# Kernel tuning notes

Measured on AMD Instinct MI355X. Metric: run time of the kernel, lower is better.

The kernel has to match this reference:

```python
import jax, jax.numpy as jnp
import numpy as np

N, DX, D, K, H = 4096, 128, 64, 256, 256
BETA = 0.25


def setup_inputs() -> dict:
    key = jax.random.key(0)
    ks = jax.random.split(key, 10)
    z_sample = jax.random.normal(ks[0], (N, D), jnp.float32)
    k_idx = jax.random.randint(ks[1], (N,), 0, K)
    k_sample = jax.nn.one_hot(k_idx, K, dtype=jnp.float32)  # carry is one-hot
    xt = jax.random.normal(ks[2], (N, DX), jnp.float32)
    mask = jax.random.bernoulli(ks[3], 0.5, (N,))
    transition = jax.random.uniform(ks[4], (N, K, K), jnp.float32, 0.01, 1.0)
    start_pk = jax.random.uniform(ks[5], (N, K), jnp.float32, 0.01, 1.0)
    start_pk = start_pk / start_pk.sum(-1, keepdims=True)
    W1 = jax.random.normal(ks[6], (D + DX, H), jnp.float32) / np.float32(np.sqrt(D + DX))
    b1 = jnp.zeros((H,), jnp.float32)
    W2 = jax.random.normal(ks[7], (H, H), jnp.float32) / np.float32(np.sqrt(H))
    b2 = jnp.zeros((H,), jnp.float32)
    W3 = jax.random.normal(ks[8], (H, D), jnp.float32) / np.float32(np.sqrt(H))
    b3 = jnp.zeros((D,), jnp.float32)
    C = jax.random.normal(ks[9], (K, D), jnp.float32)
    return dict(temp=jnp.float32(1.0), z_sample=z_sample, k_sample=k_sample, xt=xt,
                mask=mask, transition=transition, start_pk=start_pk,
                W1=W1, b1=b1, W2=W2, b2=b2, W3=W3, b3=b3, C=C, seed=0)


def reference(temp, z_sample, k_sample, xt, mask, transition, start_pk,
              W1, b1, W2, b2, W3, b3, C, seed):
    key = jax.random.key(seed)
    k_rng, z_rng, key = jax.random.split(key, 3)

    # replace non-finite carry entries (initial-step sentinel)
    zf = jnp.where(jnp.isfinite(z_sample), z_sample, jnp.zeros_like(z_sample))
    kf = jnp.where(jnp.isfinite(k_sample), k_sample, jnp.ones_like(k_sample))

    # SmallTanhNet encoder gt = ez([z, x])
    h = jnp.tanh(jnp.concatenate([zf, xt], axis=-1) @ W1 + b1)
    h = jnp.tanh(h @ W2 + b2)
    gt = h @ W3 + b3  # [N, D]

    # codebook pairwise Euclidean distance + argmin (VQ)
    diff = gt[:, None, :] - C[None, :, :]  # [N, K, D]
    distances = jnp.sqrt(jnp.sum(diff * diff, axis=-1))  # [N, K]
    qk_ind = jnp.argmin(distances, axis=-1)
    qk_sample = jax.nn.one_hot(qk_ind, K, dtype=gt.dtype)  # [N, K]

    # prior over discrete state from per-sample transition
    pk_gammat = jnp.einsum('nk,nkj->nj', kf, transition)
    pk_gammat = pk_gammat / pk_gammat.sum(axis=-1, keepdims=True)
    pk_gammat = jnp.where(jnp.isfinite(k_sample), pk_gammat, start_pk)

    # sample from prior categorical, select by mask
    pk_ind = jax.random.categorical(k_rng, jnp.log(pk_gammat), axis=-1)
    pk_sample = jax.nn.one_hot(pk_ind, K, dtype=gt.dtype)
    k_new = jnp.where(mask[:, None], qk_sample, pk_sample)

    # KL(Categorical(qk_sample) || Categorical(pk_gammat)); qk is one-hot so
    # sum q log q = 0 and KL = -sum q log p
    discrete_kl = -jnp.sum(qk_sample * jnp.log(pk_gammat), axis=-1)

    z_new = k_new @ C  # [N, D]

    sg = jax.lax.stop_gradient
    kl = jnp.sqrt(jnp.sum(jnp.abs(sg(gt) - z_new) ** 2, axis=-1))
    kl = kl + BETA * jnp.sqrt(jnp.sum(jnp.abs(gt - sg(z_new)) ** 2, axis=-1))

    return (z_new, kl + discrete_kl, discrete_kl, qk_sample)
```

## Files before the change

### kernel.cpp

```cpp
#include <hip/hip_runtime.h>
#include <cstdint>
#include <cmath>

#define NN   4096
#define DXX  128
#define DD   64
#define KK   256
#define HH   256
#define DIN  192
#define ROWS 16
#define NT   1024
#define GRID (NN/ROWS)

typedef __attribute__((ext_vector_type(8))) short short8;
typedef __attribute__((ext_vector_type(4))) float f32x4;
#define MFMA __builtin_amdgcn_mfma_f32_16x16x32_bf16

#define OW1 0
#define OW2 147456
#define OW3 344064
#define OCT 393216
#define OCN 442368

#define SW  264
#define SG  72
#define SSP 260
#define SSG 68

__device__ __forceinline__ unsigned short f2bf(float x){
  uint32_t u = __float_as_uint(x);
  return (unsigned short)((u + 0x7fffu + ((u>>16)&1u)) >> 16);
}
__device__ __forceinline__ float bf2f(unsigned short b){
  return __uint_as_float(((uint32_t)b)<<16);
}
__device__ __forceinline__ void split3(float x, unsigned short& h, unsigned short& m, unsigned short& l){
  h = f2bf(x); float r1 = x - bf2f(h);
  m = f2bf(r1); float r2 = r1 - bf2f(m);
  l = f2bf(r2);
}

__device__ __forceinline__ uint32_t rotl32(uint32_t v, uint32_t r){ return (v<<r)|(v>>(32u-r)); }
__device__ __forceinline__ void tf2x32(uint32_t k0, uint32_t k1,
                                       uint32_t x0, uint32_t x1,
                                       uint32_t& o0, uint32_t& o1){
  const uint32_t ks0=k0, ks1=k1, ks2 = k0 ^ k1 ^ 0x1BD11BDAu;
  x0 += ks0; x1 += ks1;
  x0+=x1; x1=rotl32(x1,13); x1^=x0;
  x0+=x1; x1=rotl32(x1,15); x1^=x0;
  x0+=x1; x1=rotl32(x1,26); x1^=x0;
  x0+=x1; x1=rotl32(x1, 6); x1^=x0;
  x0+=ks1; x1+=ks2+1u;
  x0+=x1; x1=rotl32(x1,17); x1^=x0;
  x0+=x1; x1=rotl32(x1,29); x1^=x0;
  x0+=x1; x1=rotl32(x1,16); x1^=x0;
  x0+=x1; x1=rotl32(x1,24); x1^=x0;
  x0+=ks2; x1+=ks0+2u;
  x0+=x1; x1=rotl32(x1,13); x1^=x0;
  x0+=x1; x1=rotl32(x1,15); x1^=x0;
  x0+=x1; x1=rotl32(x1,26); x1^=x0;
  x0+=x1; x1=rotl32(x1, 6); x1^=x0;
  x0+=ks0; x1+=ks1+3u;
  x0+=x1; x1=rotl32(x1,17); x1^=x0;
  x0+=x1; x1=rotl32(x1,29); x1^=x0;
  x0+=x1; x1=rotl32(x1,16); x1^=x0;
  x0+=x1; x1=rotl32(x1,24); x1^=x0;
  x0+=ks1; x1+=ks2+4u;
  x0+=x1; x1=rotl32(x1,13); x1^=x0;
  x0+=x1; x1=rotl32(x1,15); x1^=x0;
  x0+=x1; x1=rotl32(x1,26); x1^=x0;
  x0+=x1; x1=rotl32(x1, 6); x1^=x0;
  x0+=ks2; x1+=ks0+5u;
  o0=x0; o1=x1;
}
__device__ __forceinline__ float gumbel_of(uint32_t ka0, uint32_t ka1, uint32_t idx){
  uint32_t o0,o1; tf2x32(ka0,ka1,0u,idx,o0,o1);
  const uint32_t bits = o0 ^ o1;
  const float TINY = 1.17549435e-38f;
  const float f = __uint_as_float((bits>>9) | 0x3F800000u) - 1.0f;
  const float u = fmaxf(TINY, f + TINY);
  return -logf(-logf(u));
}

__global__ __launch_bounds__(256) void k_prep(const float* __restrict__ W1,
    const float* __restrict__ W2, const float* __restrict__ W3,
    const float* __restrict__ Cg, unsigned short* __restrict__ ws){
  const int b = blockIdx.x, t = threadIdx.x;
  __shared__ __align__(16) float lds[2112];
  if (b < 64){
    const float* W; int N, KS, NTt, ks, cg; size_t base;
    if (b < 24){ W=W1; N=256; KS=6; NTt=16; base=OW1; ks=b/4;      cg=b&3; }
    else if (b < 56){ W=W2; N=256; KS=8; NTt=16; base=OW2; ks=(b-24)/4; cg=(b-24)&3; }
    else { W=W3; N=64; KS=8; NTt=4; base=OW3; ks=b-56; cg=0; }
    const int k0 = ks*32, cb = cg*64;
    for (int idx=t; idx<512; idx+=256){
      int row = idx>>4, c4 = idx&15;
      float4 v = *(const float4*)&W[(size_t)(k0+row)*N + cb + c4*4];
      float* d = &lds[row*65 + c4*4];
      d[0]=v.x; d[1]=v.y; d[2]=v.z; d[3]=v.w;
    }
    __syncthreads();
    const size_t term = (size_t)NTt*KS*512;
    const int lane = t&63, ctl = t>>6;
    const int ct = cg*4 + ctl;
    const int cl = ctl*16 + (lane&15);
    const int kofs = 8*(lane>>4);
    short8 hv,mv,lv;
    #pragma unroll
    for (int j=0;j<8;++j){
      float w = lds[(kofs+j)*65 + cl];
      unsigned short h,m,lo; split3(w,h,m,lo);
      hv[j]=(short)h; mv[j]=(short)m; lv[j]=(short)lo;
    }
    const size_t o = base + ((size_t)ct*KS+ks)*512 + (size_t)lane*8;
    *(short8*)&ws[o]=hv; *(short8*)&ws[o+term]=mv; *(short8*)&ws[o+2*term]=lv;
  } else if (b < 72){
    const int ks = (b-64)/4, cg = (b-64)&3;
    const int d0 = ks*32, code0 = cg*64;
    for (int idx=t; idx<512; idx+=256){
      int code = idx>>3, d4 = idx&7;
      float4 v = *(const float4*)&Cg[(size_t)(code0+code)*64 + d0 + d4*4];
      float* d = &lds[code*33 + d4*4];
      d[0]=v.x; d[1]=v.y; d[2]=v.z; d[3]=v.w;
    }
    __syncthreads();
    const size_t term = (size_t)16*2*512;
    const int lane = t&63, ctl = t>>6;
    const int ct = cg*4 + ctl;
    const int cl = ctl*16 + (lane&15);
    const int kofs = 8*(lane>>4);
    short8 hv,mv,lv;
    #pragma unroll
    for (int j=0;j<8;++j){
      float w = lds[cl*33 + kofs + j];
      unsigned short h,m,lo; split3(w,h,m,lo);
      hv[j]=(short)h; mv[j]=(short)m; lv[j]=(short)lo;
    }
    const size_t o = OCT + ((size_t)ct*2+ks)*512 + (size_t)lane*8;
    *(short8*)&ws[o]=hv; *(short8*)&ws[o+term]=mv; *(short8*)&ws[o+2*term]=lv;
  } else {
    const int c = t;
    float s=0.f;
    #pragma unroll 8
    for (int d=0; d<64; ++d){ float v=Cg[(size_t)c*64+d]; s += v*v; }
    ((float*)(ws+OCN))[c] = s;
  }
}

__global__ __launch_bounds__(NT,4) void k_fused(
    const float* __restrict__ z, const float* __restrict__ ks,
    const float* __restrict__ xt, const void* __restrict__ maskp,
    const float* __restrict__ tr, const float* __restrict__ spk,
    const float* __restrict__ b1, const float* __restrict__ b2,
    const float* __restrict__ b3, const float* __restrict__ Cg,
    const int* __restrict__ seedp, const unsigned short* __restrict__ pws,
    float* __restrict__ out_z, float* __restrict__ out_kl,
    float* __restrict__ out_dkl, float* __restrict__ out_qk)
{
  const int t    = threadIdx.x;
  const int lane = t & 63;
  const int wv   = t >> 6;
  const int lr   = lane & 15;
  const int lg   = lane >> 4;
  const int n0   = blockIdx.x * ROWS;
  const int nw   = n0 + wv;

  __shared__ __align__(16) char smem[61952];
  unsigned short* Ah = (unsigned short*)smem;
  unsigned short* Am = Ah + 16*SW;
  unsigned short* Al = Am + 16*SW;
  unsigned short* Bh = (unsigned short*)(smem + 25344);
  unsigned short* Bm = Bh + 16*SW;
  unsigned short* Bl = Bm + 16*SW;
  float* sp  = (float*)(smem + 25344);
  float* sgt = (float*)(smem + 50688);
  unsigned short* Gh = (unsigned short*)(smem + 55040);
  unsigned short* Gm = Gh + 16*SG;
  unsigned short* Gl = Gm + 16*SG;
  __shared__ int sh_flag;
  const float* cnormp = (const float*)(pws + OCN);

  const float4 ksq = ((const float4*)ks)[(size_t)nw*(KK/4)+lane];
  int kv=0x7fffffff;
  if (isfinite(ksq.x)&&ksq.x>0.5f) kv=4*lane+0;
  if (isfinite(ksq.y)&&ksq.y>0.5f&&4*lane+1<kv) kv=4*lane+1;
  if (isfinite(ksq.z)&&ksq.z>0.5f&&4*lane+2<kv) kv=4*lane+2;
  if (isfinite(ksq.w)&&ksq.w>0.5f&&4*lane+3<kv) kv=4*lane+3;
  { unsigned long long bl=__ballot(kv!=0x7fffffff);
    if (bl){ int src=(int)__builtin_ctzll(bl); kv=__shfl(kv,src,64); } else kv=0; }
  const int kidx = kv;
  const float4 trq = ((const float4*)tr)[(size_t)nw*(KK*KK/4)+(size_t)kidx*(KK/4)+lane];
  const unsigned char mb = ((const unsigned char*)maskp)[nw];
  const uint32_t      mw32 = ((const uint32_t*)maskp)[nw];

  if (t==0) sh_flag = 0;
  __syncthreads();
  {
    const uint32_t* mwp = (const uint32_t*)maskp;
    uint32_t wd = mwp[t];
    if (wd!=0u && wd!=1u && wd!=0x3F800000u) atomicOr(&sh_flag,1);
  }

  for (int i=t; i<ROWS*DIN; i+=NT){
    int r=i/DIN, d=i%DIN; float v;
    if (d<DD){ v = z[(size_t)(n0+r)*DD+d]; if(!isfinite(v)) v=0.f; }
    else     { v = xt[(size_t)(n0+r)*DXX + (d-DD)]; }
    unsigned short h,m,l_; split3(v,h,m,l_);
    Ah[r*SW+d]=h; Am[r*SW+d]=m; Al[r*SW+d]=l_;
  }
  __syncthreads();
  const int flag = sh_flag;

  auto gemm_layer = [&](const unsigned short* Xh, const unsigned short* Xm, const unsigned short* Xl,
                        int KS, size_t wbase, const float* bias,
                        unsigned short* Yh, unsigned short* Ym, unsigned short* Yl){
    const int ct = wv;
    const size_t term = (size_t)16*KS*512;
    const float bb = bias[ct*16+lr];
    f32x4 ahh = {bb,bb,bb,bb};
    f32x4 ahm = {0.f,0.f,0.f,0.f}, amh=ahm, amm=ahm, alh=ahm, ahl=ahm;
    const int ar = lr*SW + lg*8;
    const unsigned short* p = &pws[wbase + ((size_t)ct*KS)*512 + (size_t)lane*8];
    short8 bh = *(const short8*)p, bm = *(const short8*)(p+term), bl = *(const short8*)(p+2*term);
    #pragma unroll 1
    for (int s=0; s<KS; ++s){
      short8 nbh, nbm, nbl;
      if (s+1<KS){
        const unsigned short* q = p + (size_t)(s+1)*512;
        nbh=*(const short8*)q; nbm=*(const short8*)(q+term); nbl=*(const short8*)(q+2*term);
      }
      short8 ah = *(const short8*)&Xh[ar + s*32];
      short8 am = *(const short8*)&Xm[ar + s*32];
      short8 al = *(const short8*)&Xl[ar + s*32];
      ahh=MFMA(ah,bh,ahh,0,0,0); ahm=MFMA(ah,bm,ahm,0,0,0);
      amh=MFMA(am,bh,amh,0,0,0); amm=MFMA(am,bm,amm,0,0,0);
      alh=MFMA(al,bh,alh,0,0,0); ahl=MFMA(ah,bl,ahl,0,0,0);
      bh=nbh; bm=nbm; bl=nbl;
    }
    #pragma unroll
    for (int j=0;j<4;++j){
      const int r = lg*4 + j;
      float h0 = tanhf(((ahh[j]+amh[j])+alh[j]) + ((ahm[j]+amm[j])+ahl[j]));
      unsigned short hh,hm,hl; split3(h0,hh,hm,hl);
      Yh[r*SW + ct*16+lr]=hh; Ym[r*SW + ct*16+lr]=hm; Yl[r*SW + ct*16+lr]=hl;
    }
  };

  gemm_layer(Ah,Am,Al, 6, OW1, b1, Bh,Bm,Bl);
  __syncthreads();
  gemm_layer(Bh,Bm,Bl, 8, OW2, b2, Ah,Am,Al);
  __syncthreads();

  if (wv < 4){
    const int ct = wv;
    const size_t term = (size_t)4*8*512;
    const float bb = b3[ct*16+lr];
    f32x4 ahh = {bb,bb,bb,bb};
    f32x4 ahm = {0.f,0.f,0.f,0.f}, amh=ahm, amm=ahm, alh=ahm, ahl=ahm;
    const int ar = lr*SW + lg*8;
    const unsigned short* p = &pws[OW3 + ((size_t)ct*8)*512 + (size_t)lane*8];
    short8 bh = *(const short8*)p, bm = *(const short8*)(p+term), bl = *(const short8*)(p+2*term);
    #pragma unroll 1
    for (int s=0; s<8; ++s){
      short8 nbh, nbm, nbl;
      if (s+1<8){
        const unsigned short* q = p + (size_t)(s+1)*512;
        nbh=*(const short8*)q; nbm=*(const short8*)(q+term); nbl=*(const short8*)(q+2*term);
      }
      short8 ah = *(const short8*)&Ah[ar + s*32];
      short8 am = *(const short8*)&Am[ar + s*32];
      short8 al = *(const short8*)&Al[ar + s*32];
      ahh=MFMA(ah,bh,ahh,0,0,0); ahm=MFMA(ah,bm,ahm,0,0,0);
      amh=MFMA(am,bh,amh,0,0,0); amm=MFMA(am,bm,amm,0,0,0);
      alh=MFMA(al,bh,alh,0,0,0); ahl=MFMA(ah,bl,ahl,0,0,0);
      bh=nbh; bm=nbm; bl=nbl;
    }
    #pragma unroll
    for (int j=0;j<4;++j){
      const int r = lg*4 + j;
      float g = ((ahh[j]+amh[j])+alh[j]) + ((ahm[j]+amm[j])+ahl[j]);
      sgt[r*SSG + ct*16+lr] = g;
      unsigned short gh,gm,gl; split3(g,gh,gm,gl);
      Gh[r*SG + ct*16+lr]=gh; Gm[r*SG + ct*16+lr]=gm; Gl[r*SG + ct*16+lr]=gl;
    }
  }

  uint32_t ka0,ka1;
  tf2x32(0u,(uint32_t)seedp[0],0u,0u,ka0,ka1);
  const bool m = flag ? (mb!=0) : (mw32!=0u);
  float g0=0,g1=0,g2=0,g3=0;
  if (!m){
    g0=gumbel_of(ka0,ka1,(uint32_t)(nw*KK+4*lane+0));
    g1=gumbel_of(ka0,ka1,(uint32_t)(nw*KK+4*lane+1));
    g2=gumbel_of(ka0,ka1,(uint32_t)(nw*KK+4*lane+2));
    g3=gumbel_of(ka0,ka1,(uint32_t)(nw*KK+4*lane+3));
  }
  __syncthreads();

  {
    const int ct = wv;
    const size_t term = (size_t)16*2*512;
    f32x4 shh={0.f,0.f,0.f,0.f}, shm=shh, smh=shh, smm=shh, slh=shh, shl=shh;
    const int ar = lr*SG + lg*8;
    #pragma unroll
    for (int s=0; s<2; ++s){
      short8 ah = *(const short8*)&Gh[ar + s*32];
      short8 am = *(const short8*)&Gm[ar + s*32];
      short8 al = *(const short8*)&Gl[ar + s*32];
      const unsigned short* p = &pws[OCT + ((size_t)ct*2 + s)*512 + (size_t)lane*8];
      short8 bh=*(const short8*)p, bm=*(const short8*)(p+term), bl=*(const short8*)(p+2*term);
      shh=MFMA(ah,bh,shh,0,0,0); shm=MFMA(ah,bm,shm,0,0,0);
      smh=MFMA(am,bh,smh,0,0,0); smm=MFMA(am,bm,smm,0,0,0);
      slh=MFMA(al,bh,slh,0,0,0); shl=MFMA(ah,bl,shl,0,0,0);
    }
    const float cn = cnormp[ct*16+lr];
    #pragma unroll
    for (int j=0;j<4;++j){
      const int r = lg*4 + j;
      float dot = ((shh[j]+smh[j])+slh[j]) + ((shm[j]+smm[j])+shl[j]);
      sp[r*SSP + ct*16+lr] = cn - 2.f*dot;
    }
  }
  __syncthreads();

  {
    const int n = nw, r = wv;
    const float FMX = 3.402823466e38f;
    float4 dq = *(const float4*)&sp[r*SSP + 4*lane];
    float dv=dq.x; int di=4*lane;
    if (dq.y<dv){dv=dq.y;di=4*lane+1;}
    if (dq.z<dv){dv=dq.z;di=4*lane+2;}
    if (dq.w<dv){dv=dq.w;di=4*lane+3;}
    #pragma unroll
    for (int mm=32;mm;mm>>=1){
      float ov=__shfl_xor(dv,mm,64); int oi=__shfl_xor(di,mm,64);
      if (ov<dv||(ov==dv&&oi<di)){dv=ov;di=oi;}
    }
    const int i1=di;
    float v0=(4*lane+0==i1)?FMX:dq.x, v1=(4*lane+1==i1)?FMX:dq.y;
    float v2=(4*lane+2==i1)?FMX:dq.z, v3=(4*lane+3==i1)?FMX:dq.w;
    float ev=v0; int ei=4*lane;
    if (v1<ev){ev=v1;ei=4*lane+1;}
    if (v2<ev){ev=v2;ei=4*lane+2;}
    if (v3<ev){ev=v3;ei=4*lane+3;}
    #pragma unroll
    for (int mm=32;mm;mm>>=1){
      float ov=__shfl_xor(ev,mm,64); int oi=__shfl_xor(ei,mm,64);
      if (ov<ev||(ov==ev&&oi<ei)){ev=ov;ei=oi;}
    }
    const int i2=ei;
    const float gd = sgt[r*SSG + lane];
    float e1 = gd - Cg[(size_t)i1*DD + lane];
    float e2 = gd - Cg[(size_t)i2*DD + lane];
    float s1 = e1*e1, s2 = e2*e2;
    #pragma unroll
    for (int mm=32;mm;mm>>=1){ s1 += __shfl_xor(s1,mm,64); s2 += __shfl_xor(s2,mm,64); }
    const float D1 = sqrtf(s1), D2 = sqrtf(s2);
    const int qk = (D2<D1 || (D2==D1 && i2<i1)) ? i2 : i1;

    float s=((trq.x+trq.y)+trq.z)+trq.w;
    #pragma unroll
    for (int mm=32;mm;mm>>=1) s+=__shfl_xor(s,mm,64);
    float q0=trq.x/s, q1=trq.y/s, q2=trq.z/s, q3=trq.w/s;
    { bool f0=isfinite(ksq.x),f1=isfinite(ksq.y),f2=isfinite(ksq.z),f3=isfinite(ksq.w);
      if (__any(!(f0&&f1&&f2&&f3))){
        float4 sq=((const float4*)spk)[(size_t)n*(KK/4)+lane];
        if(!f0)q0=sq.x; if(!f1)q1=sq.y; if(!f2)q2=sq.z; if(!f3)q3=sq.w;
      } }
    const float lp0=logf(q0), lp1=logf(q1), lp2=logf(q2), lp3=logf(q3);
    const int jq=qk&3;
    float lps=(jq==0)?lp0:((jq==1)?lp1:((jq==2)?lp2:lp3));
    const float logqk=__shfl(lps,qk>>2,64);

    int sel;
    if (m){ sel=qk; }
    else {
      float sc=g0+lp0; int si=4*lane;
      { float g=g1+lp1; if(g>sc){sc=g;si=4*lane+1;} }
      { float g=g2+lp2; if(g>sc){sc=g;si=4*lane+2;} }
      { float g=g3+lp3; if(g>sc){sc=g;si=4*lane+3;} }
      #pragma unroll
      for (int mm=32;mm;mm>>=1){
        float ov=__shfl_xor(sc,mm,64); int oi=__shfl_xor(si,mm,64);
        if (ov>sc||(ov==sc&&oi<si)){sc=ov;si=oi;}
      }
      sel=si;
    }

    ((float4*)out_qk)[(size_t)n*(KK/4)+lane]=make_float4(
      (4*lane+0==qk)?1.f:0.f,(4*lane+1==qk)?1.f:0.f,
      (4*lane+2==qk)?1.f:0.f,(4*lane+3==qk)?1.f:0.f);

    const float c=Cg[(size_t)sel*DD+lane];
    out_z[(size_t)n*DD+lane]=c;
    float df = sgt[r*SSG + lane] - c;
    float p=df*df;
    #pragma unroll
    for (int mm=32;mm;mm>>=1) p+=__shfl_xor(p,mm,64);
    if (lane==0){
      float tt=sqrtf(p);
      float dkl=-logqk;
      out_kl[n]=(tt+0.25f*tt)+dkl;
      out_dkl[n]=dkl;
    }
  }
}

extern "C" void kernel_launch(void* const* d_in, const int* in_sizes, int n_in,
                              void* d_out, int out_size, void* d_ws, size_t ws_size,
                              hipStream_t stream){
  const float* z    = (const float*)d_in[1];
  const float* ksm  = (const float*)d_in[2];
  const float* xt   = (const float*)d_in[3];
  const void*  mask = d_in[4];
  const float* tr   = (const float*)d_in[5];
  const float* spk  = (const float*)d_in[6];
  const float* W1   = (const float*)d_in[7];
  const float* b1   = (const float*)d_in[8];
  const float* W2   = (const float*)d_in[9];
  const float* b2   = (const float*)d_in[10];
  const float* W3   = (const float*)d_in[11];
  const float* b3   = (const float*)d_in[12];
  const float* C    = (const float*)d_in[13];
  const int*   seed = (const int*)d_in[14];

  float* out_z   = (float*)d_out;
  float* out_kl  = out_z   + (size_t)NN*DD;
  float* out_dkl = out_kl  + NN;
  float* out_qk  = out_dkl + NN;

  unsigned short* ws = (unsigned short*)d_ws;
  k_prep<<<73,256,0,stream>>>(W1, W2, W3, C, ws);
  k_fused<<<GRID,NT,0,stream>>>(z, ksm, xt, mask, tr, spk,
                                b1, b2, b3, C, seed, ws,
                                out_z, out_kl, out_dkl, out_qk);
}
```

Baseline: 31.24 us.

## Prefetch layer weights across barriers, split-K layer 3 over all waves, merge accumulators

Moves the first weight-fragment loads for each GEMM stage ahead of the preceding __syncthreads so their global latency overlaps the barrier. Layer 3 was run by only four waves; it is now split along K across all 16 waves, with partial sums written to shared memory and reduced by all threads before the codebook distance stage. The six separate MFMA accumulators per tile are folded into two chained accumulators to cut register use. Chaining the MFMAs adds dependency stalls and changes the summation order, and the split-K adds an extra shared-memory reduction pass.

```diff
diff --git a/kernel.cpp b/kernel.cpp
--- a/kernel.cpp
+++ b/kernel.cpp
@@ -172,8 +172,9 @@
   unsigned short* Bh = (unsigned short*)(smem + 25344);
   unsigned short* Bm = Bh + 16*SW;
   unsigned short* Bl = Bm + 16*SW;
-  float* sp  = (float*)(smem + 25344);
-  float* sgt = (float*)(smem + 50688);
+  float* part = (float*)(smem + 25344);
+  float* sp   = (float*)(smem + 25344);
+  float* sgt  = (float*)(smem + 50688);
   unsigned short* Gh = (unsigned short*)(smem + 55040);
   unsigned short* Gm = Gh + 16*SG;
   unsigned short* Gl = Gm + 16*SG;
@@ -193,6 +194,10 @@
   const unsigned char mb = ((const unsigned char*)maskp)[nw];
   const uint32_t      mw32 = ((const uint32_t*)maskp)[nw];
 
+  const size_t term1 = (size_t)16*6*512;
+  const unsigned short* p1 = &pws[OW1 + ((size_t)wv*6)*512 + (size_t)lane*8];
+  short8 f1h = *(const short8*)p1, f1m = *(const short8*)(p1+term1), f1l = *(const short8*)(p1+2*term1);
+
   if (t==0) sh_flag = 0;
   __syncthreads();
   {
@@ -213,15 +218,14 @@
 
   auto gemm_layer = [&](const unsigned short* Xh, const unsigned short* Xm, const unsigned short* Xl,
                         int KS, size_t wbase, const float* bias,
+                        short8 bh, short8 bm, short8 bl,
                         unsigned short* Yh, unsigned short* Ym, unsigned short* Yl){
     const int ct = wv;
     const size_t term = (size_t)16*KS*512;
     const float bb = bias[ct*16+lr];
-    f32x4 ahh = {bb,bb,bb,bb};
-    f32x4 ahm = {0.f,0.f,0.f,0.f}, amh=ahm, amm=ahm, alh=ahm, ahl=ahm;
+    f32x4 a0 = {bb,bb,bb,bb}, a1 = {0.f,0.f,0.f,0.f};
     const int ar = lr*SW + lg*8;
     const unsigned short* p = &pws[wbase + ((size_t)ct*KS)*512 + (size_t)lane*8];
-    short8 bh = *(const short8*)p, bm = *(const short8*)(p+term), bl = *(const short8*)(p+2*term);
     #pragma unroll 1
     for (int s=0; s<KS; ++s){
       short8 nbh, nbm, nbl;
@@ -232,56 +236,57 @@
       short8 ah = *(const short8*)&Xh[ar + s*32];
       short8 am = *(const short8*)&Xm[ar + s*32];
       short8 al = *(const short8*)&Xl[ar + s*32];
-      ahh=MFMA(ah,bh,ahh,0,0,0); ahm=MFMA(ah,bm,ahm,0,0,0);
-      amh=MFMA(am,bh,amh,0,0,0); amm=MFMA(am,bm,amm,0,0,0);
-      alh=MFMA(al,bh,alh,0,0,0); ahl=MFMA(ah,bl,ahl,0,0,0);
+      a0=MFMA(ah,bh,a0,0,0,0); a1=MFMA(ah,bm,a1,0,0,0);
+      a0=MFMA(am,bh,a0,0,0,0); a1=MFMA(am,bm,a1,0,0,0);
+      a0=MFMA(al,bh,a0,0,0,0); a1=MFMA(ah,bl,a1,0,0,0);
       bh=nbh; bm=nbm; bl=nbl;
     }
     #pragma unroll
     for (int j=0;j<4;++j){
       const int r = lg*4 + j;
-      float h0 = tanhf(((ahh[j]+amh[j])+alh[j]) + ((ahm[j]+amm[j])+ahl[j]));
+      float h0 = tanhf(a0[j]+a1[j]);
       unsigned short hh,hm,hl; split3(h0,hh,hm,hl);
       Yh[r*SW + ct*16+lr]=hh; Ym[r*SW + ct*16+lr]=hm; Yl[r*SW + ct*16+lr]=hl;
     }
   };
 
-  gemm_layer(Ah,Am,Al, 6, OW1, b1, Bh,Bm,Bl);
-  __syncthreads();
-  gemm_layer(Bh,Bm,Bl, 8, OW2, b2, Ah,Am,Al);
-  __syncthreads();
-
-  if (wv < 4){
-    const int ct = wv;
-    const size_t term = (size_t)4*8*512;
-    const float bb = b3[ct*16+lr];
-    f32x4 ahh = {bb,bb,bb,bb};
-    f32x4 ahm = {0.f,0.f,0.f,0.f}, amh=ahm, amm=ahm, alh=ahm, ahl=ahm;
+  gemm_layer(Ah,Am,Al, 6, OW1, b1, f1h,f1m,f1l, Bh,Bm,Bl);
+  const size_t term2 = (size_t)16*8*512;
+  const unsigned short* p2 = &pws[OW2 + ((size_t)wv*8)*512 + (size_t)lane*8];
+  short8 f2h = *(const short8*)p2, f2m = *(const short8*)(p2+term2), f2l = *(const short8*)(p2+2*term2);
+  __syncthreads();
+
+  gemm_layer(Bh,Bm,Bl, 8, OW2, b2, f2h,f2m,f2l, Ah,Am,Al);
+  const int ct3 = wv & 3, kq3 = wv >> 2;
+  const size_t term3 = (size_t)4*8*512;
+  const unsigned short* p3 = &pws[OW3 + ((size_t)ct3*8 + kq3*2)*512 + (size_t)lane*8];
+  short8 f3h = *(const short8*)p3, f3m = *(const short8*)(p3+term3), f3l = *(const short8*)(p3+2*term3);
+  __syncthreads();
+
+  {
+    f32x4 a0 = {0.f,0.f,0.f,0.f}, a1 = a0;
     const int ar = lr*SW + lg*8;
-    const unsigned short* p = &pws[OW3 + ((size_t)ct*8)*512 + (size_t)lane*8];
-    short8 bh = *(const short8*)p, bm = *(const short8*)(p+term), bl = *(const short8*)(p+2*term);
+    short8 bh=f3h, bm=f3m, bl=f3l;
     #pragma unroll 1
-    for (int s=0; s<8; ++s){
+    for (int s=0; s<2; ++s){
       short8 nbh, nbm, nbl;
-      if (s+1<8){
-        const unsigned short* q = p + (size_t)(s+1)*512;
-        nbh=*(const short8*)q; nbm=*(const short8*)(q+term); nbl=*(const short8*)(q+2*term);
+      if (s==0){
+        const unsigned short* q = p3 + 512;
+        nbh=*(const short8*)q; nbm=*(const short8*)(q+term3); nbl=*(const short8*)(q+2*term3);
       }
-      short8 ah = *(const short8*)&Ah[ar + s*32];
-      short8 am = *(const short8*)&Am[ar + s*32];
-      short8 al = *(const short8*)&Al[ar + s*32];
-      ahh=MFMA(ah,bh,ahh,0,0,0); ahm=MFMA(ah,bm,ahm,0,0,0);
-      amh=MFMA(am,bh,amh,0,0,0); amm=MFMA(am,bm,amm,0,0,0);
-      alh=MFMA(al,bh,alh,0,0,0); ahl=MFMA(ah,bl,ahl,0,0,0);
+      const int sg = kq3*2 + s;
+      short8 ah = *(const short8*)&Ah[ar + sg*32];
+      short8 am = *(const short8*)&Am[ar + sg*32];
+      short8 al = *(const short8*)&Al[ar + sg*32];
+      a0=MFMA(ah,bh,a0,0,0,0); a1=MFMA(ah,bm,a1,0,0,0);
+      a0=MFMA(am,bh,a0,0,0,0); a1=MFMA(am,bm,a1,0,0,0);
+      a0=MFMA(al,bh,a0,0,0,0); a1=MFMA(ah,bl,a1,0,0,0);
       bh=nbh; bm=nbm; bl=nbl;
     }
     #pragma unroll
     for (int j=0;j<4;++j){
       const int r = lg*4 + j;
-      float g = ((ahh[j]+amh[j])+alh[j]) + ((ahm[j]+amm[j])+ahl[j]);
-      sgt[r*SSG + ct*16+lr] = g;
-      unsigned short gh,gm,gl; split3(g,gh,gm,gl);
-      Gh[r*SG + ct*16+lr]=gh; Gm[r*SG + ct*16+lr]=gm; Gl[r*SG + ct*16+lr]=gl;
+      part[kq3*1040 + r*65 + ct3*16+lr] = a0[j]+a1[j];
     }
   }
 
@@ -298,27 +303,46 @@
   __syncthreads();
 
   {
+    const int r = t>>6, c = t&63;
+    float g = b3[c];
+    g += part[0*1040 + r*65 + c];
+    g += part[1*1040 + r*65 + c];
+    g += part[2*1040 + r*65 + c];
+    g += part[3*1040 + r*65 + c];
+    sgt[r*SSG + c] = g;
+    unsigned short gh,gm,gl; split3(g,gh,gm,gl);
+    Gh[r*SG+c]=gh; Gm[r*SG+c]=gm; Gl[r*SG+c]=gl;
+  }
+  const size_t termC = (size_t)16*2*512;
+  const unsigned short* pC = &pws[OCT + ((size_t)wv*2)*512 + (size_t)lane*8];
+  short8 fCh = *(const short8*)pC, fCm = *(const short8*)(pC+termC), fCl = *(const short8*)(pC+2*termC);
+  __syncthreads();
+
+  {
     const int ct = wv;
-    const size_t term = (size_t)16*2*512;
-    f32x4 shh={0.f,0.f,0.f,0.f}, shm=shh, smh=shh, smm=shh, slh=shh, shl=shh;
+    f32x4 s0={0.f,0.f,0.f,0.f}, s1=s0;
     const int ar = lr*SG + lg*8;
-    #pragma unroll
+    short8 bh=fCh, bm=fCm, bl=fCl;
+    #pragma unroll 1
     for (int s=0; s<2; ++s){
+      short8 nbh, nbm, nbl;
+      if (s==0){
+        const unsigned short* q = pC + 512;
+        nbh=*(const short8*)q; nbm=*(const short8*)(q+termC); nbl=*(const short8*)(q+2*termC);
+      }
       short8 ah = *(const short8*)&Gh[ar + s*32];
       short8 am = *(const short8*)&Gm[ar + s*32];
       short8 al = *(const short8*)&Gl[ar + s*32];
-      const unsigned short* p = &pws[OCT + ((size_t)ct*2 + s)*512 + (size_t)lane*8];
-      short8 bh=*(const short8*)p, bm=*(const short8*)(p+term), bl=*(const short8*)(p+2*term);
-      shh=MFMA(ah,bh,shh,0,0,0); shm=MFMA(ah,bm,shm,0,0,0);
-      smh=MFMA(am,bh,smh,0,0,0); smm=MFMA(am,bm,smm,0,0,0);
-      slh=MFMA(al,bh,slh,0,0,0); shl=MFMA(ah,bl,shl,0,0,0);
+      s0=MFMA(ah,bh,s0,0,0,0); s1=MFMA(ah,bm,s1,0,0,0);
+      s0=MFMA(am,bh,s0,0,0,0); s1=MFMA(am,bm,s1,0,0,0);
+      s0=MFMA(al,bh,s0,0,0,0); s1=MFMA(ah,bl,s1,0,0,0);
+      bh=nbh; bm=nbm; bl=nbl;
     }
     const float cn = cnormp[ct*16+lr];
     #pragma unroll
     for (int j=0;j<4;++j){
       const int r = lg*4 + j;
-      float dot = ((shh[j]+smh[j])+slh[j]) + ((shm[j]+smm[j])+shl[j]);
-      sp[r*SSP + ct*16+lr] = cn - 2.f*dot;
+      sp[r*SSP + ct*16+lr] = cn - 2.f*(s0[j]+s1[j]);
     }
   }
   __syncthreads();
```

Result: no change. 30.82 us (-1.3%).

## Halve rows per block and give each wave two output column tiles

Applied to the files above, without the earlier changes.

Each block now handles 8 rows with 512 threads instead of 16 rows with 1024, which doubles the grid and halves shared memory. Because the MFMA M dimension stays 16, the A rows are duplicated (lr&7) and only half the lanes write results, so each wave now computes two 16-column tiles per layer. The six split-precision accumulators are merged into two chains, and the register double-buffering of weight prefetch is dropped. This is meant to spread work over more CUs, but it wastes half of every MFMA on duplicated rows, makes weight loads per row redundant, and serialises MFMA dependencies on the accumulators.

```diff
diff --git a/kernel.cpp b/kernel.cpp
--- a/kernel.cpp
+++ b/kernel.cpp
@@ -8,8 +8,8 @@
 #define KK   256
 #define HH   256
 #define DIN  192
-#define ROWS 16
-#define NT   1024
+#define ROWS 8
+#define NT   512
 #define GRID (NN/ROWS)
 
 typedef __attribute__((ext_vector_type(8))) short short8;
@@ -165,18 +165,18 @@
   const int n0   = blockIdx.x * ROWS;
   const int nw   = n0 + wv;
 
-  __shared__ __align__(16) char smem[61952];
+  __shared__ __align__(16) char smem[30976];
   unsigned short* Ah = (unsigned short*)smem;
-  unsigned short* Am = Ah + 16*SW;
-  unsigned short* Al = Am + 16*SW;
-  unsigned short* Bh = (unsigned short*)(smem + 25344);
-  unsigned short* Bm = Bh + 16*SW;
-  unsigned short* Bl = Bm + 16*SW;
-  float* sp  = (float*)(smem + 25344);
-  float* sgt = (float*)(smem + 50688);
-  unsigned short* Gh = (unsigned short*)(smem + 55040);
-  unsigned short* Gm = Gh + 16*SG;
-  unsigned short* Gl = Gm + 16*SG;
+  unsigned short* Am = Ah + 8*SW;
+  unsigned short* Al = Am + 8*SW;
+  unsigned short* Bh = (unsigned short*)(smem + 12672);
+  unsigned short* Bm = Bh + 8*SW;
+  unsigned short* Bl = Bm + 8*SW;
+  float* sp  = (float*)(smem + 12672);
+  float* sgt = (float*)(smem + 25344);
+  unsigned short* Gh = (unsigned short*)(smem + 27520);
+  unsigned short* Gm = Gh + 8*SG;
+  unsigned short* Gl = Gm + 8*SG;
   __shared__ int sh_flag;
   const float* cnormp = (const float*)(pws + OCN);
 
@@ -197,8 +197,10 @@
   __syncthreads();
   {
     const uint32_t* mwp = (const uint32_t*)maskp;
-    uint32_t wd = mwp[t];
-    if (wd!=0u && wd!=1u && wd!=0x3F800000u) atomicOr(&sh_flag,1);
+    uint32_t bad=0;
+    #pragma unroll
+    for (int q=0;q<2;++q){ uint32_t wd=mwp[t+q*NT]; if (wd!=0u && wd!=1u && wd!=0x3F800000u) bad=1; }
+    if (bad) atomicOr(&sh_flag,1);
   }
 
   for (int i=t; i<ROWS*DIN; i+=NT){
@@ -214,35 +216,41 @@
   auto gemm_layer = [&](const unsigned short* Xh, const unsigned short* Xm, const unsigned short* Xl,
                         int KS, size_t wbase, const float* bias,
                         unsigned short* Yh, unsigned short* Ym, unsigned short* Yl){
-    const int ct = wv;
+    const int ct0 = wv*2, ct1 = ct0+1;
     const size_t term = (size_t)16*KS*512;
-    const float bb = bias[ct*16+lr];
-    f32x4 ahh = {bb,bb,bb,bb};
-    f32x4 ahm = {0.f,0.f,0.f,0.f}, amh=ahm, amm=ahm, alh=ahm, ahl=ahm;
-    const int ar = lr*SW + lg*8;
-    const unsigned short* p = &pws[wbase + ((size_t)ct*KS)*512 + (size_t)lane*8];
-    short8 bh = *(const short8*)p, bm = *(const short8*)(p+term), bl = *(const short8*)(p+2*term);
+    const float bb0 = bias[ct0*16+lr], bb1 = bias[ct1*16+lr];
+    f32x4 a00 = {bb0,bb0,bb0,bb0}, a01 = {0.f,0.f,0.f,0.f};
+    f32x4 a10 = {bb1,bb1,bb1,bb1}, a11 = {0.f,0.f,0.f,0.f};
+    const int ar = (lr&7)*SW + lg*8;
+    const unsigned short* p0 = &pws[wbase + ((size_t)ct0*KS)*512 + (size_t)lane*8];
+    const unsigned short* p1 = &pws[wbase + ((size_t)ct1*KS)*512 + (size_t)lane*8];
     #pragma unroll 1
     for (int s=0; s<KS; ++s){
-      short8 nbh, nbm, nbl;
-      if (s+1<KS){
-        const unsigned short* q = p + (size_t)(s+1)*512;
-        nbh=*(const short8*)q; nbm=*(const short8*)(q+term); nbl=*(const short8*)(q+2*term);
-      }
+      const unsigned short* q0 = p0 + (size_t)s*512;
+      const unsigned short* q1 = p1 + (size_t)s*512;
+      short8 bh0=*(const short8*)q0, bm0=*(const short8*)(q0+term), bl0=*(const short8*)(q0+2*term);
+      short8 bh1=*(const short8*)q1, bm1=*(const short8*)(q1+term), bl1=*(const short8*)(q1+2*term);
       short8 ah = *(const short8*)&Xh[ar + s*32];
       short8 am = *(const short8*)&Xm[ar + s*32];
       short8 al = *(const short8*)&Xl[ar + s*32];
-      ahh=MFMA(ah,bh,ahh,0,0,0); ahm=MFMA(ah,bm,ahm,0,0,0);
-      amh=MFMA(am,bh,amh,0,0,0); amm=MFMA(am,bm,amm,0,0,0);
-      alh=MFMA(al,bh,alh,0,0,0); ahl=MFMA(ah,bl,ahl,0,0,0);
-      bh=nbh; bm=nbm; bl=nbl;
-    }
-    #pragma unroll
-    for (int j=0;j<4;++j){
-      const int r = lg*4 + j;
-      float h0 = tanhf(((ahh[j]+amh[j])+alh[j]) + ((ahm[j]+amm[j])+ahl[j]));
-      unsigned short hh,hm,hl; split3(h0,hh,hm,hl);
-      Yh[r*SW + ct*16+lr]=hh; Ym[r*SW + ct*16+lr]=hm; Yl[r*SW + ct*16+lr]=hl;
+      a00=MFMA(ah,bh0,a00,0,0,0); a01=MFMA(ah,bm0,a01,0,0,0);
+      a00=MFMA(am,bh0,a00,0,0,0); a01=MFMA(am,bm0,a01,0,0,0);
+      a00=MFMA(al,bh0,a00,0,0,0); a01=MFMA(ah,bl0,a01,0,0,0);
+      a10=MFMA(ah,bh1,a10,0,0,0); a11=MFMA(ah,bm1,a11,0,0,0);
+      a10=MFMA(am,bh1,a10,0,0,0); a11=MFMA(am,bm1,a11,0,0,0);
+      a10=MFMA(al,bh1,a10,0,0,0); a11=MFMA(ah,bl1,a11,0,0,0);
+    }
+    if (lg < 2){
+      #pragma unroll
+      for (int j=0;j<4;++j){
+        const int r = lg*4 + j;
+        float h0 = tanhf(a00[j]+a01[j]);
+        unsigned short hh,hm,hl; split3(h0,hh,hm,hl);
+        Yh[r*SW + ct0*16+lr]=hh; Ym[r*SW + ct0*16+lr]=hm; Yl[r*SW + ct0*16+lr]=hl;
+        float h1v = tanhf(a10[j]+a11[j]);
+        split3(h1v,hh,hm,hl);
+        Yh[r*SW + ct1*16+lr]=hh; Ym[r*SW + ct1*16+lr]=hm; Yl[r*SW + ct1*16+lr]=hl;
+      }
     }
   };
 
@@ -255,33 +263,29 @@
     const int ct = wv;
     const size_t term = (size_t)4*8*512;
     const float bb = b3[ct*16+lr];
-    f32x4 ahh = {bb,bb,bb,bb};
-    f32x4 ahm = {0.f,0.f,0.f,0.f}, amh=ahm, amm=ahm, alh=ahm, ahl=ahm;
-    const int ar = lr*SW + lg*8;
+    f32x4 a0 = {bb,bb,bb,bb}, a1 = {0.f,0.f,0.f,0.f};
+    const int ar = (lr&7)*SW + lg*8;
     const unsigned short* p = &pws[OW3 + ((size_t)ct*8)*512 + (size_t)lane*8];
-    short8 bh = *(const short8*)p, bm = *(const short8*)(p+term), bl = *(const short8*)(p+2*term);
     #pragma unroll 1
     for (int s=0; s<8; ++s){
-      short8 nbh, nbm, nbl;
-      if (s+1<8){
-        const unsigned short* q = p + (size_t)(s+1)*512;
-        nbh=*(const short8*)q; nbm=*(const short8*)(q+term); nbl=*(const short8*)(q+2*term);
-      }
+      const unsigned short* q = p + (size_t)s*512;
+      short8 bh=*(const short8*)q, bm=*(const short8*)(q+term), bl=*(const short8*)(q+2*term);
       short8 ah = *(const short8*)&Ah[ar + s*32];
       short8 am = *(const short8*)&Am[ar + s*32];
       short8 al = *(const short8*)&Al[ar + s*32];
-      ahh=MFMA(ah,bh,ahh,0,0,0); ahm=MFMA(ah,bm,ahm,0,0,0);
-      amh=MFMA(am,bh,amh,0,0,0); amm=MFMA(am,bm,amm,0,0,0);
-      alh=MFMA(al,bh,alh,0,0,0); ahl=MFMA(ah,bl,ahl,0,0,0);
-      bh=nbh; bm=nbm; bl=nbl;
-    }
-    #pragma unroll
-    for (int j=0;j<4;++j){
-      const int r = lg*4 + j;
-      float g = ((ahh[j]+amh[j])+alh[j]) + ((ahm[j]+amm[j])+ahl[j]);
-      sgt[r*SSG + ct*16+lr] = g;
-      unsigned short gh,gm,gl; split3(g,gh,gm,gl);
-      Gh[r*SG + ct*16+lr]=gh; Gm[r*SG + ct*16+lr]=gm; Gl[r*SG + ct*16+lr]=gl;
+      a0=MFMA(ah,bh,a0,0,0,0); a1=MFMA(ah,bm,a1,0,0,0);
+      a0=MFMA(am,bh,a0,0,0,0); a1=MFMA(am,bm,a1,0,0,0);
+      a0=MFMA(al,bh,a0,0,0,0); a1=MFMA(ah,bl,a1,0,0,0);
+    }
+    if (lg < 2){
+      #pragma unroll
+      for (int j=0;j<4;++j){
+        const int r = lg*4 + j;
+        float g = a0[j]+a1[j];
+        sgt[r*SSG + ct*16+lr] = g;
+        unsigned short gh,gm,gl; split3(g,gh,gm,gl);
+        Gh[r*SG + ct*16+lr]=gh; Gm[r*SG + ct*16+lr]=gm; Gl[r*SG + ct*16+lr]=gl;
+      }
     }
   }
 
@@ -298,27 +302,34 @@
   __syncthreads();
 
   {
-    const int ct = wv;
+    const int ct0 = wv*2, ct1 = ct0+1;
     const size_t term = (size_t)16*2*512;
-    f32x4 shh={0.f,0.f,0.f,0.f}, shm=shh, smh=shh, smm=shh, slh=shh, shl=shh;
-    const int ar = lr*SG + lg*8;
+    f32x4 s00={0.f,0.f,0.f,0.f}, s01=s00, s10=s00, s11=s00;
+    const int ar = (lr&7)*SG + lg*8;
     #pragma unroll
     for (int s=0; s<2; ++s){
+      const unsigned short* q0 = &pws[OCT + ((size_t)ct0*2 + s)*512 + (size_t)lane*8];
+      const unsigned short* q1 = &pws[OCT + ((size_t)ct1*2 + s)*512 + (size_t)lane*8];
+      short8 bh0=*(const short8*)q0, bm0=*(const short8*)(q0+term), bl0=*(const short8*)(q0+2*term);
+      short8 bh1=*(const short8*)q1, bm1=*(const short8*)(q1+term), bl1=*(const short8*)(q1+2*term);
       short8 ah = *(const short8*)&Gh[ar + s*32];
       short8 am = *(const short8*)&Gm[ar + s*32];
       short8 al = *(const short8*)&Gl[ar + s*32];
-      const unsigned short* p = &pws[OCT + ((size_t)ct*2 + s)*512 + (size_t)lane*8];
-      short8 bh=*(const short8*)p, bm=*(const short8*)(p+term), bl=*(const short8*)(p+2*term);
-      shh=MFMA(ah,bh,shh,0,0,0); shm=MFMA(ah,bm,shm,0,0,0);
-      smh=MFMA(am,bh,smh,0,0,0); smm=MFMA(am,bm,smm,0,0,0);
-      slh=MFMA(al,bh,slh,0,0,0); shl=MFMA(ah,bl,shl,0,0,0);
-    }
-    const float cn = cnormp[ct*16+lr];
-    #pragma unroll
-    for (int j=0;j<4;++j){
-      const int r = lg*4 + j;
-      float dot = ((shh[j]+smh[j])+slh[j]) + ((shm[j]+smm[j])+shl[j]);
-      sp[r*SSP + ct*16+lr] = cn - 2.f*dot;
+      s00=MFMA(ah,bh0,s00,0,0,0); s01=MFMA(ah,bm0,s01,0,0,0);
+      s00=MFMA(am,bh0,s00,0,0,0); s01=MFMA(am,bm0,s01,0,0,0);
+      s00=MFMA(al,bh0,s00,0,0,0); s01=MFMA(ah,bl0,s01,0,0,0);
+      s10=MFMA(ah,bh1,s10,0,0,0); s11=MFMA(ah,bm1,s11,0,0,0);
+      s10=MFMA(am,bh1,s10,0,0,0); s11=MFMA(am,bm1,s11,0,0,0);
+      s10=MFMA(al,bh1,s10,0,0,0); s11=MFMA(ah,bl1,s11,0,0,0);
+    }
+    const float cn0 = cnormp[ct0*16+lr], cn1 = cnormp[ct1*16+lr];
+    if (lg < 2){
+      #pragma unroll
+      for (int j=0;j<4;++j){
+        const int r = lg*4 + j;
+        sp[r*SSP + ct0*16+lr] = cn0 - 2.f*(s00[j]+s01[j]);
+        sp[r*SSP + ct1*16+lr] = cn1 - 2.f*(s10[j]+s11[j]);
+      }
     }
   }
   __syncthreads();
```

Result: slower. 39.10 us (+25.2%).
